# Performance work log

Measured on AMD Instinct MI355X. Metric: run time of the kernel, lower is better.

Reference implementation:

```python
import jax, jax.numpy as jnp
import numpy as np
from jax import lax

KERNEL_SIZE = 2
DILATION = 1


def setup_inputs() -> dict:
    key = jax.random.key(0)
    k1, k2, k3, k4, k5 = jax.random.split(key, 5)
    bsz, h_size, seq_len = 8, 1024, 1024
    z1ss = jax.random.normal(k1, (bsz, 2 * h_size, seq_len), dtype=jnp.float32)
    uss = jax.random.normal(k2, (bsz, 4 * h_size, seq_len), dtype=jnp.float32)
    z0 = jax.random.normal(k3, (bsz, 2 * h_size, 1), dtype=jnp.float32)
    # conv params initialized ~ N(0, 0.01) as in init_weights
    weight = 0.01 * jax.random.normal(k4, (4 * h_size, h_size, KERNEL_SIZE), dtype=jnp.float32)
    bias = 0.01 * jax.random.normal(k5, (4 * h_size,), dtype=jnp.float32)
    return {"z1ss": z1ss, "uss": uss, "z0": z0, "weight": weight, "bias": bias}


def reference(z1ss, uss, z0, weight, bias):
    h_size = z1ss.shape[1] // 2
    z1h, z1c = z1ss[:, :h_size], z1ss[:, h_size:]          # (B, H, T) each
    z0h, z0c0 = z0[:, :h_size], z0[:, h_size:]             # (B, H, 1)
    # previous cell state: [z0c, z1c[..., :-1]]
    z0c = jnp.concatenate([z0c0, z1c], axis=2)[:, :, :-1]  # (B, H, T)
    # causal pad, injecting hid into the padded region
    pad = (KERNEL_SIZE - 1) * DILATION
    b = z1h.shape[0]
    hid = jnp.broadcast_to(z0h, (b, h_size, pad))
    xp = jnp.concatenate([hid, z1h], axis=2)               # (B, H, T+pad)
    conv = lax.conv_general_dilated(
        xp, weight, window_strides=(1,), padding='VALID',
        rhs_dilation=(DILATION,), dimension_numbers=('NCH', 'OIH', 'NCH'))
    out = uss + conv + bias[None, :, None]                 # (B, 4H, T)
    it, ot, gt, ft = jnp.split(out, 4, axis=1)
    it, ot, gt, ft = jax.nn.sigmoid(it), jax.nn.sigmoid(ot), jnp.tanh(gt), jax.nn.sigmoid(ft)
    ct = ft * z0c + it * gt
    ht = ot * jnp.tanh(ct)
    return jnp.concatenate([ht, ct], axis=1)               # (B, 2H, T)
```

## Files before the change

### kernel.cpp

```cpp
#include <hip/hip_runtime.h>
#include <hip/hip_bf16.h>
#include <cstdint>

#define HSZ   1024
#define SEQ   1024
#define NTOT  8192
#define K2    2048

typedef __attribute__((ext_vector_type(8))) short bf16x8;
typedef __attribute__((ext_vector_type(4))) float f32x4;

__device__ __forceinline__ unsigned f2bf(float x) {
  unsigned u = __builtin_bit_cast(unsigned, x);
  return (u + 0x7fffu + ((u >> 16) & 1u)) >> 16;
}
__device__ __forceinline__ float fsig(float x)  { return 1.f / (1.f + __expf(-x)); }
__device__ __forceinline__ float ftanh(float x) { return 1.f - 2.f / (__expf(2.f * x) + 1.f); }

__device__ __forceinline__ void gload_lds16(const void* g, void* l) {
  __builtin_amdgcn_global_load_lds(
      (const __attribute__((address_space(1))) unsigned*)g,
      (__attribute__((address_space(3))) unsigned*)l, 16, 0, 0);
}

__global__ void conv_weight_kernel(const float* __restrict__ w, unsigned* __restrict__ wb) {
  const int idx = (blockIdx.x * 256 + threadIdx.x) * 8;
  const int o  = idx >> 11;
  const int kk = idx & 2047;
  const int g = o >> 10, c = o & 1023;
  const int R = (c << 2) | g;
  f32x4 a = *(const f32x4*)(w + idx);
  f32x4 d = *(const f32x4*)(w + idx + 4);
  uint4 ov;
  ov.x = f2bf(a.x) | (f2bf(a.y) << 16);
  ov.y = f2bf(a.z) | (f2bf(a.w) << 16);
  ov.z = f2bf(d.x) | (f2bf(d.y) << 16);
  ov.w = f2bf(d.z) | (f2bf(d.w) << 16);
  *(uint4*)(wb + (((R << 11) | kk) >> 1)) = ov;
}

__global__ void build_bdup_kernel(const float* __restrict__ z1ss, const float* __restrict__ z0,
                                  unsigned* __restrict__ bd) {
  __shared__ float tile[32 * 65];
  const int tid = threadIdx.x;
  const int n0 = blockIdx.x * 64;
  const int i0 = blockIdx.y * 32;
  const int b  = n0 >> 10;
  const int t0 = n0 & 1023;
  const int l16 = tid & 15, r16 = tid >> 4;
#pragma unroll
  for (int pr = 0; pr < 2; ++pr) {
    const int ii = r16 + pr * 16;
    const float* zrow = z1ss + (size_t)(b * 2048 + i0 + ii) * 1024;
    f32x4 v = *(const f32x4*)(zrow + t0 + l16 * 4);
    float* tr = tile + ii * 65 + 1 + l16 * 4;
    tr[0] = v.x; tr[1] = v.y; tr[2] = v.z; tr[3] = v.w;
    if (l16 == 0)
      tile[ii * 65] = t0 ? zrow[t0 - 1] : z0[b * 2048 + i0 + ii];
  }
  __syncthreads();
  const int i2 = tid & 31, ts = tid >> 5;
#pragma unroll
  for (int p = 0; p < 8; ++p) {
    const int tt = ts + p * 8;
    float prev = tile[i2 * 65 + tt];
    float cur  = tile[i2 * 65 + tt + 1];
    bd[(size_t)(n0 + tt) * 1024 + i0 + i2] = f2bf(prev) | (f2bf(cur) << 16);
  }
}

__launch_bounds__(256, 3)
__global__ void lstm_gemm_kernel(const unsigned short* __restrict__ Wb,
                                 const unsigned short* __restrict__ Bd,
                                 const float* __restrict__ uss,
                                 const float* __restrict__ z1ss,
                                 const float* __restrict__ z0,
                                 const float* __restrict__ bias,
                                 float* __restrict__ out) {
  __shared__ unsigned short Asm_[128 * 64];
  __shared__ unsigned short Bsm_[128 * 64];
  const int tid  = threadIdx.x;
  const int wave = tid >> 6, lane = tid & 63;
  const int l15  = lane & 15, quad = lane >> 4;
  const int wm   = wave >> 1, wn = wave & 1;
  const int c0 = blockIdx.y * 32;
  const int n0 = blockIdx.x * 128;

  const unsigned short* agp[4];
  const unsigned short* bgp[4];
#pragma unroll
  for (int j = 0; j < 4; ++j) {
    const int idx = (wave * 4 + j) * 64 + lane;
    const int row = idx >> 3;
    const int chunk = (idx & 7) ^ (row & 7);
    agp[j] = Wb + (size_t)(c0 * 4 + row) * K2 + chunk * 8;
    bgp[j] = Bd + (size_t)(n0 + row) * K2 + chunk * 8;
  }
  unsigned short* ldsA[4];
  unsigned short* ldsB[4];
#pragma unroll
  for (int j = 0; j < 4; ++j) {
    ldsA[j] = Asm_ + (wave * 4 + j) * 512;
    ldsB[j] = Bsm_ + (wave * 4 + j) * 512;
  }

  const int sw7 = l15 & 7;

  f32x4 acc[4][4];
#pragma unroll
  for (int m = 0; m < 4; ++m)
#pragma unroll
    for (int nt = 0; nt < 4; ++nt)
      acc[m][nt] = (f32x4){0.f, 0.f, 0.f, 0.f};

  for (int k0 = 0; k0 < K2; k0 += 64) {
#pragma unroll
    for (int j = 0; j < 4; ++j) gload_lds16(agp[j] + k0, ldsA[j]);
#pragma unroll
    for (int j = 0; j < 4; ++j) gload_lds16(bgp[j] + k0, ldsB[j]);
    __syncthreads();

#pragma unroll
    for (int kh = 0; kh < 2; ++kh) {
      const int slot = ((kh * 4 + quad) ^ sw7) << 3;
      bf16x8 bf[4];
#pragma unroll
      for (int nt = 0; nt < 4; ++nt)
        bf[nt] = *(const bf16x8*)(Bsm_ + (wn * 64 + nt * 16 + l15) * 64 + slot);
#pragma unroll
      for (int m = 0; m < 4; ++m) {
        bf16x8 af = *(const bf16x8*)(Asm_ + (wm * 64 + m * 16 + l15) * 64 + slot);
#pragma unroll
        for (int nt = 0; nt < 4; ++nt)
          acc[m][nt] = __builtin_amdgcn_mfma_f32_16x16x32_bf16(af, bf[nt], acc[m][nt], 0, 0, 0);
      }
    }
    __syncthreads();
  }

#pragma unroll
  for (int m = 0; m < 4; ++m) {
    const int ch = c0 + wm * 16 + m * 4 + quad;
    const float bv0 = bias[ch], bv1 = bias[1024 + ch], bv2 = bias[2048 + ch], bv3 = bias[3072 + ch];
#pragma unroll
    for (int nt = 0; nt < 4; ++nt) {
      const int n = n0 + wn * 64 + nt * 16 + l15;
      const int b = n >> 10, t = n & 1023;
      const int ub = b * 4194304 + ch * 1024 + t;
      f32x4 ac = acc[m][nt];
      float p0 = ac.x + uss[ub]           + bv0;
      float p1 = ac.y + uss[ub + 1048576] + bv1;
      float p2 = ac.z + uss[ub + 2097152] + bv2;
      float p3 = ac.w + uss[ub + 3145728] + bv3;
      float it = fsig(p0), ot = fsig(p1), g_ = ftanh(p2), ft = fsig(p3);
      float zc = t ? z1ss[(b * 2048 + 1024 + ch) * 1024 + t - 1]
                   : z0[b * 2048 + 1024 + ch];
      float ct = ft * zc + it * g_;
      float ht = ot * ftanh(ct);
      const int ob = (b * 2048 + ch) * 1024 + t;
      out[ob] = ht;
      out[ob + 1048576] = ct;
    }
  }
}

__global__ void naive_kernel(const float* __restrict__ z1ss, const float* __restrict__ uss,
                             const float* __restrict__ z0, const float* __restrict__ w,
                             const float* __restrict__ bias, float* __restrict__ out) {
  int idx = blockIdx.x * 256 + threadIdx.x;
  int b = idx >> 20, c = (idx >> 10) & 1023, t = idx & 1023;
  float s0 = 0.f, s1 = 0.f, s2 = 0.f, s3 = 0.f;
  const float* xb = z1ss + b * 2097152;
  for (int i = 0; i < 1024; ++i) {
    float cur  = xb[i * 1024 + t];
    float prev = t ? xb[i * 1024 + t - 1] : z0[b * 2048 + i];
    const float* wr = w + c * 2048 + i * 2;
    s0 += wr[0]       * prev + wr[1]       * cur;
    s1 += wr[2097152] * prev + wr[2097153] * cur;
    s2 += wr[4194304] * prev + wr[4194305] * cur;
    s3 += wr[6291456] * prev + wr[6291457] * cur;
  }
  int ub = b * 4194304 + c * 1024 + t;
  float p0 = s0 + uss[ub]           + bias[c];
  float p1 = s1 + uss[ub + 1048576] + bias[1024 + c];
  float p2 = s2 + uss[ub + 2097152] + bias[2048 + c];
  float p3 = s3 + uss[ub + 3145728] + bias[3072 + c];
  float it = fsig(p0), ot = fsig(p1), g_ = ftanh(p2), ft = fsig(p3);
  float zc = t ? z1ss[(b * 2048 + 1024 + c) * 1024 + t - 1] : z0[b * 2048 + 1024 + c];
  float ct = ft * zc + it * g_;
  float ht = ot * ftanh(ct);
  int ob = (b * 2048 + c) * 1024 + t;
  out[ob] = ht;
  out[ob + 1048576] = ct;
}

extern "C" void kernel_launch(void* const* d_in, const int* in_sizes, int n_in,
                              void* d_out, int out_size, void* d_ws, size_t ws_size,
                              hipStream_t stream) {
  const float* z1ss = (const float*)d_in[0];
  const float* uss  = (const float*)d_in[1];
  const float* z0   = (const float*)d_in[2];
  const float* w    = (const float*)d_in[3];
  const float* bias = (const float*)d_in[4];
  float* out = (float*)d_out;

  const size_t needWb = (size_t)4096 * 2048 * 2;
  const size_t needBd = (size_t)NTOT * K2 * 2;
  if (ws_size >= needWb + needBd) {
    unsigned short* Wb = (unsigned short*)d_ws;
    unsigned short* Bd = Wb + (size_t)4096 * 2048;
    conv_weight_kernel<<<4096, 256, 0, stream>>>(w, (unsigned*)Wb);
    build_bdup_kernel<<<dim3(128, 32), 256, 0, stream>>>(z1ss, z0, (unsigned*)Bd);
    lstm_gemm_kernel<<<dim3(64, 32), 256, 0, stream>>>(Wb, Bd, uss, z1ss, z0, bias, out);
  } else {
    naive_kernel<<<32768, 256, 0, stream>>>(z1ss, uss, z0, w, bias, out);
  }
}
```

Before: 397.8 us.

## Double-buffer LDS tiles with K=32 stages to overlap loads and MFMA

Replaces the single-buffered K=64 LDS tile loop with two K=32 buffers, issuing the global-to-LDS load for the next stage before computing the current one. This removes one barrier per iteration and is meant to hide global load latency behind the MFMA work. LDS size stays the same, but the swizzle changes to a 4-chunk pattern and the loop now runs twice as many steps with shorter K, which could add barrier overhead or LDS bank conflicts.

```diff
diff --git a/kernel.cpp b/kernel.cpp
--- a/kernel.cpp
+++ b/kernel.cpp
@@ -77,8 +77,8 @@
                                  const float* __restrict__ z0,
                                  const float* __restrict__ bias,
                                  float* __restrict__ out) {
-  __shared__ unsigned short Asm_[128 * 64];
-  __shared__ unsigned short Bsm_[128 * 64];
+  __shared__ unsigned short Asm_[2 * 128 * 32];
+  __shared__ unsigned short Bsm_[2 * 128 * 32];
   const int tid  = threadIdx.x;
   const int wave = tid >> 6, lane = tid & 63;
   const int l15  = lane & 15, quad = lane >> 4;
@@ -86,25 +86,19 @@
   const int c0 = blockIdx.y * 32;
   const int n0 = blockIdx.x * 128;
 
-  const unsigned short* agp[4];
-  const unsigned short* bgp[4];
-#pragma unroll
-  for (int j = 0; j < 4; ++j) {
-    const int idx = (wave * 4 + j) * 64 + lane;
-    const int row = idx >> 3;
-    const int chunk = (idx & 7) ^ (row & 7);
-    agp[j] = Wb + (size_t)(c0 * 4 + row) * K2 + chunk * 8;
-    bgp[j] = Bd + (size_t)(n0 + row) * K2 + chunk * 8;
-  }
-  unsigned short* ldsA[4];
-  unsigned short* ldsB[4];
-#pragma unroll
-  for (int j = 0; j < 4; ++j) {
-    ldsA[j] = Asm_ + (wave * 4 + j) * 512;
-    ldsB[j] = Bsm_ + (wave * 4 + j) * 512;
-  }
-
-  const int sw7 = l15 & 7;
+  const unsigned short *aG[2], *bG[2];
+  int sOfs[2];
+#pragma unroll
+  for (int j = 0; j < 2; ++j) {
+    const int u = (wave * 2 + j) * 64 + lane;
+    const int row = u >> 2;
+    const int ck = ((u & 3) ^ ((row >> 1) & 3)) * 8;
+    aG[j] = Wb + (size_t)(c0 * 4 + row) * K2 + ck;
+    bG[j] = Bd + (size_t)(n0 + row) * K2 + ck;
+    sOfs[j] = (wave * 2 + j) * 512;
+  }
+
+  const int slot = ((quad ^ ((l15 >> 1) & 3)) << 3);
 
   f32x4 acc[4][4];
 #pragma unroll
@@ -113,30 +107,43 @@
     for (int nt = 0; nt < 4; ++nt)
       acc[m][nt] = (f32x4){0.f, 0.f, 0.f, 0.f};
 
-  for (int k0 = 0; k0 < K2; k0 += 64) {
-#pragma unroll
-    for (int j = 0; j < 4; ++j) gload_lds16(agp[j] + k0, ldsA[j]);
-#pragma unroll
-    for (int j = 0; j < 4; ++j) gload_lds16(bgp[j] + k0, ldsB[j]);
+  auto stage = [&](int buf, int k0) {
+#pragma unroll
+    for (int j = 0; j < 2; ++j) gload_lds16(aG[j] + k0, Asm_ + buf * 4096 + sOfs[j]);
+#pragma unroll
+    for (int j = 0; j < 2; ++j) gload_lds16(bG[j] + k0, Bsm_ + buf * 4096 + sOfs[j]);
+  };
+  auto compute = [&](int buf) {
+    const unsigned short* At = Asm_ + buf * 4096;
+    const unsigned short* Bt = Bsm_ + buf * 4096;
+    bf16x8 bf[4];
+#pragma unroll
+    for (int nt = 0; nt < 4; ++nt)
+      bf[nt] = *(const bf16x8*)(Bt + (wn * 64 + nt * 16 + l15) * 32 + slot);
+#pragma unroll
+    for (int m = 0; m < 4; ++m) {
+      bf16x8 af = *(const bf16x8*)(At + (wm * 64 + m * 16 + l15) * 32 + slot);
+#pragma unroll
+      for (int nt = 0; nt < 4; ++nt)
+        acc[m][nt] = __builtin_amdgcn_mfma_f32_16x16x32_bf16(af, bf[nt], acc[m][nt], 0, 0, 0);
+    }
+  };
+
+  stage(0, 0);
+  __syncthreads();
+
+  for (int t = 0; t < 62; t += 2) {
+    stage(1, (t + 1) * 32);
+    compute(0);
     __syncthreads();
-
-#pragma unroll
-    for (int kh = 0; kh < 2; ++kh) {
-      const int slot = ((kh * 4 + quad) ^ sw7) << 3;
-      bf16x8 bf[4];
-#pragma unroll
-      for (int nt = 0; nt < 4; ++nt)
-        bf[nt] = *(const bf16x8*)(Bsm_ + (wn * 64 + nt * 16 + l15) * 64 + slot);
-#pragma unroll
-      for (int m = 0; m < 4; ++m) {
-        bf16x8 af = *(const bf16x8*)(Asm_ + (wm * 64 + m * 16 + l15) * 64 + slot);
-#pragma unroll
-        for (int nt = 0; nt < 4; ++nt)
-          acc[m][nt] = __builtin_amdgcn_mfma_f32_16x16x32_bf16(af, bf[nt], acc[m][nt], 0, 0, 0);
-      }
-    }
+    stage(0, (t + 2) * 32);
+    compute(1);
     __syncthreads();
   }
+  stage(1, 63 * 32);
+  compute(0);
+  __syncthreads();
+  compute(1);
 
 #pragma unroll
   for (int m = 0; m < 4; ++m) {
```

Measured after the change: 434.2 us. 9.2% more time.
